# Optimization experiments

Measured on AMD Instinct MI355X. Metric: run time of the kernel, lower is better.

## Reference

```python
import jax, jax.numpy as jnp
import numpy as np


def setup_inputs() -> dict:
    key = jax.random.key(0)
    k1, k2, k3, k4 = jax.random.split(key, 4)
    B, S, D, F = 16, 4096, 1024, 1024
    x = jax.random.normal(k1, (B, S, D), dtype=jnp.float32)
    # Keras 'normal' initializer ~ N(0, 0.05); scale similarly for realism
    W_key = jax.random.normal(k2, (D, F), dtype=jnp.float32) * 0.05
    W_query = jax.random.normal(k3, (D, F), dtype=jnp.float32) * 0.05
    W_value = jax.random.normal(k4, (D, F), dtype=jnp.float32) * 0.05
    return {"x": x, "W_key": W_key, "W_query": W_query, "W_value": W_value}


def reference(x, W_key, W_query, W_value):
    # x: [B,S,D]; W_*: [D,F]
    keys = jnp.tanh(jnp.einsum("bsd,df->bsf", x, W_key))
    query = jnp.tanh(jnp.einsum("bsd,df->bsf", x, W_query))
    value = jnp.tanh(jnp.einsum("bsd,df->bsf", x, W_value))
    # diag(Q K^T) == per-token dot product, computed directly in O(S*F)
    attn_scores = jnp.einsum("bsf,bsf->bs", query, keys)  # [B,S]
    attn_softmax = jax.nn.softmax(attn_scores, axis=-1)[..., None]  # [B,S,1]
    # value^T @ softmax -> [B,F,1]
    weighted_input = jnp.einsum("bsf,bso->bfo", value, attn_softmax)
    return weighted_input, attn_softmax
```

## Files before the change

kernel.cpp:

```cpp
#include <hip/hip_runtime.h>
#include <hip/hip_bf16.h>
#include <math.h>
#include <stdint.h>

typedef _Float16 f16;
typedef _Float16 half8 __attribute__((ext_vector_type(8)));
typedef float f32x4 __attribute__((ext_vector_type(4)));

#define B_ 16
#define S_ 4096
#define D_ 1024
#define F_ 1024
#define TOK (B_*S_)
#define TB3 128
#define FB3 64
#define NFB3 16
#define NT3 32
#define NSV 4
#define CSV (S_/NSV)

__device__ __forceinline__ void gload_lds16(const void* g, void* l) {
    __builtin_amdgcn_global_load_lds(
        (__attribute__((address_space(1))) const unsigned int*)(unsigned long long)(uintptr_t)g,
        (__attribute__((address_space(3))) unsigned int*)(unsigned int)(uintptr_t)l,
        16, 0, 0);
}

__device__ __forceinline__ void fma4(float4& a, float s, const float4& wv) {
    a.x += s * wv.x; a.y += s * wv.y; a.z += s * wv.z; a.w += s * wv.w;
}
__device__ __forceinline__ void wtanh4(float4& acc, float pw, const float4& a) {
    acc.x += pw * tanhf(a.x); acc.y += pw * tanhf(a.y);
    acc.z += pw * tanhf(a.z); acc.w += pw * tanhf(a.w);
}

__global__ void cvt_x(const float* __restrict__ x, f16* __restrict__ xh) {
    size_t i = ((size_t)blockIdx.x * 256 + threadIdx.x) * 8;
    float4 a = *(const float4*)(x + i);
    float4 b = *(const float4*)(x + i + 4);
    half8 h = {(f16)a.x,(f16)a.y,(f16)a.z,(f16)a.w,
               (f16)b.x,(f16)b.y,(f16)b.z,(f16)b.w};
    *(half8*)(xh + i) = h;
}

__global__ void cvt_w(const float* __restrict__ Wk, const float* __restrict__ Wq,
                      f16* __restrict__ wt) {
    __shared__ float tile[32][33];
    const float* W = (blockIdx.z == 0) ? Wk : Wq;
    f16* outp = wt + (size_t)blockIdx.z * D_ * F_;
    int x0 = blockIdx.x * 32, y0 = blockIdx.y * 32;
    int tx = threadIdx.x, ty = threadIdx.y;
#pragma unroll
    for (int i = 0; i < 4; i++)
        tile[ty + i*8][tx] = W[(size_t)(y0 + ty + i*8) * F_ + x0 + tx];
    __syncthreads();
#pragma unroll
    for (int i = 0; i < 4; i++)
        outp[(size_t)(x0 + ty + i*8) * D_ + y0 + tx] = (f16)tile[tx][ty + i*8];
}

__launch_bounds__(256, 3)
__global__ void score_gemm(const f16* __restrict__ xh, const f16* __restrict__ wt,
                           float* __restrict__ part) {
    __shared__ __align__(16) f16 Xs[3][TB3 * 32];
    __shared__ __align__(16) f16 Ks[3][FB3 * 32];
    __shared__ __align__(16) f16 Qs[3][FB3 * 32];
    __shared__ float sred[2][TB3];

    const int hid  = blockIdx.x + blockIdx.y * NFB3;
    const int orig = (hid & 7) * 1024 + (hid >> 3);
    const int fb   = orig & 15;
    const int f0   = fb * FB3;
    const int tok0 = (orig >> 4) * TB3;

    const int t = threadIdx.x, lane = t & 63, w = t >> 6;
    const int wr = (w >> 1) * 64;
    const int wc = (w & 1) * 32;

    const f16* wK = wt + (size_t)f0 * D_;
    const f16* wQ = wt + (size_t)D_ * F_ + (size_t)f0 * D_;

    const int rx0 = t >> 2,         qx0 = (t & 3) ^ ((rx0 >> 1) & 3);
    const int rx1 = (t + 256) >> 2, qx1 = (t & 3) ^ ((rx1 >> 1) & 3);
    const f16* srcX0 = xh + (size_t)(tok0 + rx0) * D_ + qx0 * 8;
    const f16* srcX1 = xh + (size_t)(tok0 + rx1) * D_ + qx1 * 8;
    const int rw = t >> 2,          qw = (t & 3) ^ ((rw >> 1) & 3);
    const f16* srcK = wK + (size_t)rw * D_ + qw * 8;
    const f16* srcQ = wQ + (size_t)rw * D_ + qw * 8;
    const int wbase = w * 1024;

    int offA[4], offB[2];
#pragma unroll
    for (int m = 0; m < 4; ++m) {
        int row = wr + m * 16 + (lane & 15);
        int q   = (lane >> 4) ^ ((row >> 1) & 3);
        offA[m] = row * 32 + q * 8;
    }
#pragma unroll
    for (int n = 0; n < 2; ++n) {
        int row = wc + n * 16 + (lane & 15);
        int q   = (lane >> 4) ^ ((row >> 1) & 3);
        offB[n] = row * 32 + q * 8;
    }

#define STAGE(sl, kof) do {                                           \
        gload_lds16(srcX0 + (kof), (char*)Xs[sl] + wbase);            \
        gload_lds16(srcX1 + (kof), (char*)Xs[sl] + 4096 + wbase);     \
        gload_lds16(srcK  + (kof), (char*)Ks[sl] + wbase);            \
        gload_lds16(srcQ  + (kof), (char*)Qs[sl] + wbase);            \
    } while (0)

    f32x4 accK[4][2] = {};
    f32x4 accQ[4][2] = {};

    STAGE(0, 0);
    STAGE(1, 32);
    asm volatile("s_waitcnt vmcnt(4)" ::: "memory");
    __builtin_amdgcn_s_barrier();

#pragma unroll 1
    for (int kt = 0; kt < NT3; ++kt) {
        const int cur = kt % 3;
        if (kt < NT3 - 2) {
            const int nxt = (kt + 2) % 3;
            STAGE(nxt, (kt + 2) * 32);
        }
        const f16* Xb = Xs[cur];
        const f16* Kb = Ks[cur];
        const f16* Qb = Qs[cur];

        half8 aF[4], bKf[2], bQf[2];
#pragma unroll
        for (int m = 0; m < 4; ++m) aF[m]  = *(const half8*)(Xb + offA[m]);
#pragma unroll
        for (int n = 0; n < 2; ++n) {
            bKf[n] = *(const half8*)(Kb + offB[n]);
            bQf[n] = *(const half8*)(Qb + offB[n]);
        }
#pragma unroll
        for (int n = 0; n < 2; ++n)
#pragma unroll
            for (int m = 0; m < 4; ++m) {
                accK[m][n] = __builtin_amdgcn_mfma_f32_16x16x32_f16(aF[m], bKf[n], accK[m][n], 0, 0, 0);
                accQ[m][n] = __builtin_amdgcn_mfma_f32_16x16x32_f16(aF[m], bQf[n], accQ[m][n], 0, 0, 0);
            }

        if (kt < NT3 - 2) {
            asm volatile("s_waitcnt vmcnt(4)" ::: "memory");
        } else if (kt == NT3 - 2) {
            asm volatile("s_waitcnt vmcnt(0)" ::: "memory");
        }
        if (kt < NT3 - 1) __builtin_amdgcn_s_barrier();
    }
#undef STAGE

#pragma unroll
    for (int m = 0; m < 4; ++m) {
        float s[4] = {0.f, 0.f, 0.f, 0.f};
#pragma unroll
        for (int n = 0; n < 2; ++n)
#pragma unroll
            for (int j = 0; j < 4; ++j)
                s[j] += tanhf(accQ[m][n][j]) * tanhf(accK[m][n][j]);
#pragma unroll
        for (int j = 0; j < 4; ++j) {
            s[j] += __shfl_xor(s[j], 1);
            s[j] += __shfl_xor(s[j], 2);
            s[j] += __shfl_xor(s[j], 4);
            s[j] += __shfl_xor(s[j], 8);
        }
        if ((lane & 15) == 0) {
            int g = lane >> 4;
#pragma unroll
            for (int j = 0; j < 4; ++j)
                sred[w & 1][wr + m * 16 + g * 4 + j] = s[j];
        }
    }
    __syncthreads();
    if (t < TB3)
        part[(size_t)fb * TOK + tok0 + t] = sred[0][t] + sred[1][t];
}

__global__ void softmax_k(const float* __restrict__ part, float* __restrict__ out) {
    __shared__ float sc[S_];
    __shared__ float red[256];
    const int b = blockIdx.x, t = threadIdx.x;
    float lmax = -1e30f;
    for (int i = t; i < S_; i += 256) {
        float s = 0.f;
#pragma unroll
        for (int fb = 0; fb < NFB3; ++fb) s += part[(size_t)fb * TOK + b * S_ + i];
        sc[i] = s;
        lmax = fmaxf(lmax, s);
    }
    red[t] = lmax; __syncthreads();
    for (int o = 128; o > 0; o >>= 1) { if (t < o) red[t] = fmaxf(red[t], red[t + o]); __syncthreads(); }
    const float mx = red[0]; __syncthreads();
    float lsum = 0.f;
    for (int i = t; i < S_; i += 256) { float e = expf(sc[i] - mx); sc[i] = e; lsum += e; }
    red[t] = lsum; __syncthreads();
    for (int o = 128; o > 0; o >>= 1) { if (t < o) red[t] += red[t + o]; __syncthreads(); }
    const float inv = 1.0f / red[0];
    for (int i = t; i < S_; i += 256)
        out[(size_t)B_ * F_ + (size_t)b * S_ + i] = sc[i] * inv;
}

__launch_bounds__(256)
__global__ void value_k4(const float* __restrict__ x, const float* __restrict__ Wv,
                         const float* __restrict__ p_in, float* __restrict__ vpart) {
    __shared__ __align__(16) float xs[8][D_];
    __shared__ float ps[CSV];
    __shared__ int   idxs[CSV];
    __shared__ int   wsum[4];
    __shared__ int   rbase_s;
    const int b = blockIdx.x, c = blockIdx.y;
    const int t = threadIdx.x, lane = t & 63, w = t >> 6;
    const int s0 = c * CSV;

    if (t == 0) rbase_s = 0;
    __syncthreads();
#pragma unroll 1
    for (int r = 0; r < 4; ++r) {
        int i = r * 256 + t;
        float p = p_in[(size_t)b * S_ + s0 + i];
        bool flag = p > 1e-7f;
        unsigned long long mask = __ballot(flag);
        if (lane == 0) wsum[w] = __popcll(mask);
        __syncthreads();
        int base = rbase_s;
#pragma unroll
        for (int k = 0; k < 4; ++k) if (k < w) base += wsum[k];
        if (flag) {
            int pos = base + __popcll(mask & ((1ull << lane) - 1ull));
            idxs[pos] = s0 + i;
            ps[pos] = p;
        }
        __syncthreads();
        if (t == 0) rbase_s += wsum[0] + wsum[1] + wsum[2] + wsum[3];
        __syncthreads();
    }
    const int cnt = rbase_s;

    float4 acc = {0.f, 0.f, 0.f, 0.f};
    for (int g = 0; g < cnt; g += 8) {
        __syncthreads();
#pragma unroll
        for (int r = 0; r < 8; ++r) {
            float4 v = {0.f, 0.f, 0.f, 0.f};
            if (g + r < cnt)
                v = ((const float4*)(x + ((size_t)b * S_ + idxs[g + r]) * D_))[t];
            ((float4*)xs[r])[t] = v;
        }
        __syncthreads();
        float4 a[8] = {};
#pragma unroll 2
        for (int dq = 0; dq < D_ / 4; ++dq) {
            const float* wrp = Wv + (size_t)dq * 4 * F_;
            float4 wv0 = ((const float4*)(wrp        ))[t];
            float4 wv1 = ((const float4*)(wrp + F_   ))[t];
            float4 wv2 = ((const float4*)(wrp + 2*F_ ))[t];
            float4 wv3 = ((const float4*)(wrp + 3*F_ ))[t];
#pragma unroll
            for (int r = 0; r < 8; ++r) {
                float4 xr = ((const float4*)xs[r])[dq];
                fma4(a[r], xr.x, wv0); fma4(a[r], xr.y, wv1);
                fma4(a[r], xr.z, wv2); fma4(a[r], xr.w, wv3);
            }
        }
#pragma unroll
        for (int r = 0; r < 8; ++r)
            if (g + r < cnt) wtanh4(acc, ps[g + r], a[r]);
    }
    ((float4*)(vpart + ((size_t)c * B_ + b) * F_))[t] = acc;
}

__global__ void value_red(const float* __restrict__ vpart, float* __restrict__ out) {
    int i = blockIdx.x * 256 + threadIdx.x;
    float s = 0.f;
#pragma unroll
    for (int c = 0; c < NSV; ++c) s += vpart[(size_t)c * B_ * F_ + i];
    out[i] = s;
}

extern "C" void kernel_launch(void* const* d_in, const int* in_sizes, int n_in,
                              void* d_out, int out_size, void* d_ws, size_t ws_size,
                              hipStream_t stream) {
    const float* x  = (const float*)d_in[0];
    const float* Wk = (const float*)d_in[1];
    const float* Wq = (const float*)d_in[2];
    const float* Wv = (const float*)d_in[3];
    float* out = (float*)d_out;
    char* ws = (char*)d_ws;

    f16*   xh   = (f16*)ws;
    f16*   wt   = (f16*)(ws + (size_t)TOK * D_ * 2);
    float* part = (float*)(ws + (size_t)TOK * D_ * 2 + 2 * (size_t)D_ * F_ * 2);

    cvt_x<<<TOK * D_ / 8 / 256, 256, 0, stream>>>(x, xh);
    cvt_w<<<dim3(32, 32, 2), dim3(32, 8), 0, stream>>>(Wk, Wq, wt);
    score_gemm<<<dim3(NFB3, TOK / TB3), 256, 0, stream>>>(xh, wt, part);
    softmax_k<<<B_, 256, 0, stream>>>(part, out);
    float* vpart = part;
    const float* p_in = out + (size_t)B_ * F_;
    value_k4<<<dim3(B_, NSV), 256, 0, stream>>>(x, Wv, p_in, vpart);
    value_red<<<B_ * F_ / 256, 256, 0, stream>>>(vpart, out);
}
```

Before: 600.1 us.

## Pre-swizzle weights into MFMA fragment layout and load them directly to registers

Weights are now converted into a fragment-ordered layout so each wave loads its K/Q MFMA B-operands straight from global memory into registers, double-buffered one k-step ahead. LDS staging then holds only X, which moves to a 4-deep ring, and the main loop is fully unrolled. The block index mapping is also changed so consecutive blocks share the same feature block and walk across token tiles. This aims to cut LDS traffic and ds_read pressure for the weights, at the cost of relying on the hardware to order global loads, since the explicit vmcnt waits inside the loop are removed and register pressure rises.

```diff
diff --git a/kernel.cpp b/kernel.cpp
--- a/kernel.cpp
+++ b/kernel.cpp
@@ -43,116 +43,97 @@
     *(half8*)(xh + i) = h;
 }
 
-__global__ void cvt_w(const float* __restrict__ Wk, const float* __restrict__ Wq,
-                      f16* __restrict__ wt) {
-    __shared__ float tile[32][33];
-    const float* W = (blockIdx.z == 0) ? Wk : Wq;
-    f16* outp = wt + (size_t)blockIdx.z * D_ * F_;
-    int x0 = blockIdx.x * 32, y0 = blockIdx.y * 32;
-    int tx = threadIdx.x, ty = threadIdx.y;
-#pragma unroll
-    for (int i = 0; i < 4; i++)
-        tile[ty + i*8][tx] = W[(size_t)(y0 + ty + i*8) * F_ + x0 + tx];
-    __syncthreads();
-#pragma unroll
-    for (int i = 0; i < 4; i++)
-        outp[(size_t)(x0 + ty + i*8) * D_ + y0 + tx] = (f16)tile[tx][ty + i*8];
+__global__ void cvt_w2(const float* __restrict__ Wk, const float* __restrict__ Wq,
+                       f16* __restrict__ wtf) {
+    const int gw   = blockIdx.x * 4 + (threadIdx.x >> 6);
+    const int lane = threadIdx.x & 63;
+    const int nblk = gw & 3, kt = (gw >> 2) & 31, fb = (gw >> 7) & 15, mat = gw >> 11;
+    const float* W = mat ? Wq : Wk;
+    const int f  = fb * 64 + nblk * 16 + (lane & 15);
+    const int d0 = kt * 32 + (lane >> 4) * 8;
+    half8 h;
+#pragma unroll
+    for (int e = 0; e < 8; ++e) h[e] = (f16)W[(size_t)(d0 + e) * F_ + f];
+    *(half8*)(wtf + (size_t)gw * 512 + lane * 8) = h;
 }
 
 __launch_bounds__(256, 3)
-__global__ void score_gemm(const f16* __restrict__ xh, const f16* __restrict__ wt,
+__global__ void score_gemm(const f16* __restrict__ xh, const f16* __restrict__ wtf,
                            float* __restrict__ part) {
-    __shared__ __align__(16) f16 Xs[3][TB3 * 32];
-    __shared__ __align__(16) f16 Ks[3][FB3 * 32];
-    __shared__ __align__(16) f16 Qs[3][FB3 * 32];
+    __shared__ __align__(16) f16 Xs[4][TB3 * 32];
     __shared__ float sred[2][TB3];
 
-    const int hid  = blockIdx.x + blockIdx.y * NFB3;
+    const int hid  = blockIdx.x;
     const int orig = (hid & 7) * 1024 + (hid >> 3);
-    const int fb   = orig & 15;
-    const int f0   = fb * FB3;
-    const int tok0 = (orig >> 4) * TB3;
+    const int fb   = orig >> 9;
+    const int tok0 = (orig & 511) * TB3;
 
     const int t = threadIdx.x, lane = t & 63, w = t >> 6;
     const int wr = (w >> 1) * 64;
     const int wc = (w & 1) * 32;
-
-    const f16* wK = wt + (size_t)f0 * D_;
-    const f16* wQ = wt + (size_t)D_ * F_ + (size_t)f0 * D_;
 
     const int rx0 = t >> 2,         qx0 = (t & 3) ^ ((rx0 >> 1) & 3);
     const int rx1 = (t + 256) >> 2, qx1 = (t & 3) ^ ((rx1 >> 1) & 3);
     const f16* srcX0 = xh + (size_t)(tok0 + rx0) * D_ + qx0 * 8;
     const f16* srcX1 = xh + (size_t)(tok0 + rx1) * D_ + qx1 * 8;
-    const int rw = t >> 2,          qw = (t & 3) ^ ((rw >> 1) & 3);
-    const f16* srcK = wK + (size_t)rw * D_ + qw * 8;
-    const f16* srcQ = wQ + (size_t)rw * D_ + qw * 8;
     const int wbase = w * 1024;
 
-    int offA[4], offB[2];
+    int offA[4];
 #pragma unroll
     for (int m = 0; m < 4; ++m) {
         int row = wr + m * 16 + (lane & 15);
         int q   = (lane >> 4) ^ ((row >> 1) & 3);
         offA[m] = row * 32 + q * 8;
     }
-#pragma unroll
-    for (int n = 0; n < 2; ++n) {
-        int row = wc + n * 16 + (lane & 15);
-        int q   = (lane >> 4) ^ ((row >> 1) & 3);
-        offB[n] = row * 32 + q * 8;
-    }
-
-#define STAGE(sl, kof) do {                                           \
+
+    const f16* bK = wtf + (((size_t)fb * NT3 * 4) + 2 * (w & 1)) * 512 + lane * 8;
+    const f16* bQ = bK + (size_t)NFB3 * NT3 * 4 * 512;
+
+#define STAGE_X(sl, kof) do {                                         \
         gload_lds16(srcX0 + (kof), (char*)Xs[sl] + wbase);            \
         gload_lds16(srcX1 + (kof), (char*)Xs[sl] + 4096 + wbase);     \
-        gload_lds16(srcK  + (kof), (char*)Ks[sl] + wbase);            \
-        gload_lds16(srcQ  + (kof), (char*)Qs[sl] + wbase);            \
     } while (0)
 
     f32x4 accK[4][2] = {};
     f32x4 accQ[4][2] = {};
-
-    STAGE(0, 0);
-    STAGE(1, 32);
-    asm volatile("s_waitcnt vmcnt(4)" ::: "memory");
+    half8 wKf[2][2], wQf[2][2];
+
+    STAGE_X(0, 0);
+    STAGE_X(1, 32);
+    STAGE_X(2, 64);
+#pragma unroll
+    for (int n = 0; n < 2; ++n) {
+        wKf[0][n] = *(const half8*)(bK + n * 512);
+        wQf[0][n] = *(const half8*)(bQ + n * 512);
+    }
+    asm volatile("s_waitcnt vmcnt(8)" ::: "memory");
     __builtin_amdgcn_s_barrier();
 
-#pragma unroll 1
+#pragma unroll
     for (int kt = 0; kt < NT3; ++kt) {
-        const int cur = kt % 3;
-        if (kt < NT3 - 2) {
-            const int nxt = (kt + 2) % 3;
-            STAGE(nxt, (kt + 2) * 32);
-        }
-        const f16* Xb = Xs[cur];
-        const f16* Kb = Ks[cur];
-        const f16* Qb = Qs[cur];
-
-        half8 aF[4], bKf[2], bQf[2];
-#pragma unroll
-        for (int m = 0; m < 4; ++m) aF[m]  = *(const half8*)(Xb + offA[m]);
-#pragma unroll
-        for (int n = 0; n < 2; ++n) {
-            bKf[n] = *(const half8*)(Kb + offB[n]);
-            bQf[n] = *(const half8*)(Qb + offB[n]);
-        }
+        const int cur = kt & 3, par = kt & 1, nx = par ^ 1;
+        if (kt < NT3 - 1) {
+#pragma unroll
+            for (int n = 0; n < 2; ++n) {
+                wKf[nx][n] = *(const half8*)(bK + ((size_t)(kt + 1) * 4 + n) * 512);
+                wQf[nx][n] = *(const half8*)(bQ + ((size_t)(kt + 1) * 4 + n) * 512);
+            }
+        }
+        if (kt < NT3 - 3) STAGE_X((kt + 3) & 3, (kt + 3) * 32);
+
+        half8 aF[4];
+#pragma unroll
+        for (int m = 0; m < 4; ++m) aF[m] = *(const half8*)(Xs[cur] + offA[m]);
 #pragma unroll
         for (int n = 0; n < 2; ++n)
 #pragma unroll
             for (int m = 0; m < 4; ++m) {
-                accK[m][n] = __builtin_amdgcn_mfma_f32_16x16x32_f16(aF[m], bKf[n], accK[m][n], 0, 0, 0);
-                accQ[m][n] = __builtin_amdgcn_mfma_f32_16x16x32_f16(aF[m], bQf[n], accQ[m][n], 0, 0, 0);
+                accK[m][n] = __builtin_amdgcn_mfma_f32_16x16x32_f16(aF[m], wKf[par][n], accK[m][n], 0, 0, 0);
+                accQ[m][n] = __builtin_amdgcn_mfma_f32_16x16x32_f16(aF[m], wQf[par][n], accQ[m][n], 0, 0, 0);
             }
-
-        if (kt < NT3 - 2) {
-            asm volatile("s_waitcnt vmcnt(4)" ::: "memory");
-        } else if (kt == NT3 - 2) {
-            asm volatile("s_waitcnt vmcnt(0)" ::: "memory");
-        }
         if (kt < NT3 - 1) __builtin_amdgcn_s_barrier();
     }
-#undef STAGE
+#undef STAGE_X
 
 #pragma unroll
     for (int m = 0; m < 4; ++m) {
@@ -293,12 +274,12 @@
     char* ws = (char*)d_ws;
 
     f16*   xh   = (f16*)ws;
-    f16*   wt   = (f16*)(ws + (size_t)TOK * D_ * 2);
+    f16*   wtf  = (f16*)(ws + (size_t)TOK * D_ * 2);
     float* part = (float*)(ws + (size_t)TOK * D_ * 2 + 2 * (size_t)D_ * F_ * 2);
 
     cvt_x<<<TOK * D_ / 8 / 256, 256, 0, stream>>>(x, xh);
-    cvt_w<<<dim3(32, 32, 2), dim3(32, 8), 0, stream>>>(Wk, Wq, wt);
-    score_gemm<<<dim3(NFB3, TOK / TB3), 256, 0, stream>>>(xh, wt, part);
+    cvt_w2<<<1024, 256, 0, stream>>>(Wk, Wq, wtf);
+    score_gemm<<<NFB3 * (TOK / TB3), 256, 0, stream>>>(xh, wtf, part);
     softmax_k<<<B_, 256, 0, stream>>>(part, out);
     float* vpart = part;
     const float* p_in = out + (size_t)B_ * F_;
```

After: 590.1 us. No clear change (-1.7%).
